# Optimization experiments

Hardware: AMD Instinct MI355X
Metric: run time of the kernel (lower is better)

## Reference

```python
import jax, jax.numpy as jnp
import numpy as np

N_NODES = 200000
N_EDGES = 6400000


def setup_inputs() -> dict:
    key = jax.random.key(0)
    ks = jax.random.split(key, 6)
    x = jax.random.normal(ks[0], (N_NODES, 11), dtype=jnp.float32)
    edge_index = jax.random.randint(ks[1], (2, N_EDGES), 0, N_NODES, dtype=jnp.int64)
    # orthogonal-ish init approximated by scaled gaussian; math path is identical
    W1 = jax.random.normal(ks[2], (11, 11), dtype=jnp.float32) / jnp.sqrt(11.0)
    W2 = jax.random.normal(ks[3], (11, 11), dtype=jnp.float32) / jnp.sqrt(11.0)
    W3 = jax.random.normal(ks[4], (11, 16), dtype=jnp.float32) / jnp.sqrt(11.0)
    b1 = jnp.zeros((11,), jnp.float32)
    b2 = jnp.zeros((11,), jnp.float32)
    b3 = jnp.zeros((16,), jnp.float32)
    return {"x": x, "edge_index": edge_index, "W1": W1, "b1": b1,
            "W2": W2, "b2": b2, "W3": W3, "b3": b3}


def gcn_conv(x, W, b, src, dst, n):
    """PyG GCNConv with add_self_loops=True, symmetric normalization.
    out_i = sum_{j->i} d_j^{-1/2} d_i^{-1/2} (x_j W) + d_i^{-1} (x_i W) + b
    where d includes the self-loop (+1).
    """
    h = x @ W                                                  # [N, F_out]
    deg = jax.ops.segment_sum(jnp.ones(src.shape[0], h.dtype), dst,
                              num_segments=n) + 1.0            # self-loop
    dinv = jax.lax.rsqrt(deg)                                  # [N]
    norm = dinv[src] * dinv[dst]                               # [E]
    agg = jax.ops.segment_sum(norm[:, None] * h[src], dst, num_segments=n)
    agg = agg + (dinv * dinv)[:, None] * h                     # self-loop term
    return agg + b


def reference(x, edge_index, W1, b1, W2, b2, W3, b3):
    n = x.shape[0]
    src, dst = edge_index[0], edge_index[1]
    h = jax.nn.relu(gcn_conv(x, W1, b1, src, dst, n))   # dropout p=0.0 -> identity
    h = jax.nn.relu(gcn_conv(h, W2, b2, src, dst, n))
    return gcn_conv(h, W3, b3, src, dst, n)
```

## Files before the change

kernel.cpp:

```cpp
#include <hip/hip_runtime.h>

#define N_NODES 200000
#define N_EDGES 6400000

constexpr int BSHIFT = 9;
constexpr int NBUCK  = (N_NODES + 511) / 512;
constexpr int CHUNK  = 16384;
constexpr int NCHUNK = (N_EDGES + CHUNK - 1) / CHUNK;
constexpr int MAXBUCK = 18432;
constexpr int SEGSTRIDE = 2052;
constexpr int SEGMAX = 1536;

__device__ __forceinline__ int ld_edge(const void* ei, int is64, int idx) {
    return is64 ? (int)((const long long*)ei)[idx] : ((const int*)ei)[idx];
}

__global__ void k_init(int* __restrict__ cursor, const unsigned int* __restrict__ ei,
                       int* __restrict__ flag, int* __restrict__ accG) {
    __shared__ int nz;
    int i = blockIdx.x * blockDim.x + threadIdx.x;
    if (i < N_NODES * 16) accG[i] = 0;
    if (blockIdx.x == 0) {
        int t = threadIdx.x;
        for (int j = t; j < NBUCK; j += 256) cursor[j] = j * MAXBUCK;
        if (t == 0) nz = 0;
        __syncthreads();
        if (ei[2 * t + 1] != 0u) atomicOr(&nz, 1);
        __syncthreads();
        if (t == 0) *flag = nz ? 0 : 1;
    }
}

__global__ void __launch_bounds__(1024)
k_binscatter(const void* __restrict__ ei, const int* __restrict__ flag,
             int* __restrict__ bucketCursor, unsigned int* __restrict__ bin) {
    __shared__ int hist[NBUCK];
    __shared__ int pref[NBUCK + 1];
    __shared__ int cur[NBUCK];
    __shared__ int gb[NBUCK];
    __shared__ int sc[512];
    __shared__ unsigned int stage[CHUNK];
    const int is64 = *flag;
    int b = blockIdx.x, t = threadIdx.x;
    int e0 = b * CHUNK;
    int n = min(CHUNK, N_EDGES - e0);
    for (int i = t; i < NBUCK; i += 1024) hist[i] = 0;
    int sd[16], ss[16];
#pragma unroll
    for (int j = 0; j < 16; ++j) {
        int idx = t + (j << 10);
        if (idx < n) {
            ss[j] = ld_edge(ei, is64, e0 + idx);
            sd[j] = ld_edge(ei, is64, N_EDGES + e0 + idx);
        } else {
            ss[j] = -1; sd[j] = -1;
        }
    }
    __syncthreads();
#pragma unroll
    for (int j = 0; j < 16; ++j)
        if (sd[j] >= 0) atomicAdd(&hist[sd[j] >> BSHIFT], 1);
    __syncthreads();
    if (t < 256) {
        sc[t]       = (t < NBUCK)       ? hist[t]       : 0;
        sc[t + 256] = (t + 256 < NBUCK) ? hist[t + 256] : 0;
    }
    __syncthreads();
    for (int off = 1; off < 512; off <<= 1) {
        int a0 = 0, a1 = 0;
        if (t < 256) {
            a0 = (t >= off) ? sc[t - off] : 0;
            a1 = sc[t + 256 - off];
        }
        __syncthreads();
        if (t < 256) { sc[t] += a0; sc[t + 256] += a1; }
        __syncthreads();
    }
    for (int i = t; i < NBUCK; i += 1024) {
        int excl = sc[i] - hist[i];
        pref[i] = excl;
        cur[i] = excl;
    }
    if (t == 0) pref[NBUCK] = n;
    __syncthreads();
#pragma unroll
    for (int j = 0; j < 16; ++j) {
        if (sd[j] >= 0) {
            int bk = sd[j] >> BSHIFT;
            unsigned int q = (unsigned int)ss[j] / 50000u;
            int p = atomicAdd(&cur[bk], 1);
            stage[p] = (q << 27) | ((unsigned int)(sd[j] & 511) << 18) | (unsigned int)ss[j];
        }
    }
    __syncthreads();
    for (int i = t; i < NBUCK; i += 1024) {
        int c = hist[i];
        gb[i] = c ? atomicAdd(&bucketCursor[i], c) : 0;
    }
    __syncthreads();
    int wave = t >> 6, lane = t & 63;
    for (int i = wave; i < NBUCK; i += 16) {
        int c = hist[i];
        if (!c) continue;
        int gg = gb[i];
        int room = (i + 1) * MAXBUCK - gg;
        int lim = min(c, max(room, 0));
        int pp = pref[i];
        for (int j = lane; j < lim; j += 64) bin[gg + j] = stage[pp + j];
    }
}

__global__ void __launch_bounds__(1024)
k_bucketsort(const int* __restrict__ bucketCursor, unsigned int* __restrict__ bin,
             float* __restrict__ dinv, unsigned short* __restrict__ seg16) {
    __shared__ int cnt[2048];
    __shared__ int cur[2048];
    __shared__ int tsum[1024];
    __shared__ unsigned int payload[MAXBUCK];
    int b = blockIdx.x, t = threadIdx.x;
    int base = b * MAXBUCK;
    int n = min(bucketCursor[b] - base, MAXBUCK);
    cnt[t] = 0; cnt[t + 1024] = 0;
    __syncthreads();
    for (int i = t; i < n; i += 1024) {
        unsigned int u = bin[base + i];
        int key = (int)((u >> 27) << 9) | (int)((u >> 18) & 511u);
        atomicAdd(&cnt[key], 1);
    }
    __syncthreads();
    int b0 = t * 2;
    int s = cnt[b0] + cnt[b0 + 1];
    tsum[t] = s;
    __syncthreads();
    int v = s;
    for (int off = 1; off < 1024; off <<= 1) {
        int add = (t >= off) ? tsum[t - off] : 0;
        __syncthreads();
        tsum[t] += add;
        __syncthreads();
    }
    int run = tsum[t] - v;
    cur[b0] = run;
    cur[b0 + 1] = run + cnt[b0];
    __syncthreads();
    for (int i = t; i < 2048; i += 1024)
        seg16[b * SEGSTRIDE + i] = (unsigned short)cur[i];
    if (t == 0) seg16[b * SEGSTRIDE + 2048] = (unsigned short)n;
    int node0 = b << BSHIFT;
    if (t < 512) {
        int node = node0 + t;
        if (node < N_NODES) {
            int deg = cnt[t] + cnt[512 + t] + cnt[1024 + t] + cnt[1536 + t];
            dinv[node] = rsqrtf((float)deg + 1.0f);
        }
    }
    __syncthreads();
    for (int i = t; i < n; i += 1024) {
        unsigned int u = bin[base + i];
        int key = (int)((u >> 27) << 9) | (int)((u >> 18) & 511u);
        int p = atomicAdd(&cur[key], 1);
        if (p < MAXBUCK) payload[p] = (u & 0x3FFFFu) << 4;
    }
    __syncthreads();
    for (int i = t; i < n; i += 1024) bin[base + i] = payload[i];
}

template <int FIN, int FOUT, int SIN>
__global__ void k_xw(const float* xin, const float* __restrict__ W,
                     const float* __restrict__ dinv, float* hs) {
    __shared__ float sW[FIN * FOUT];
    int t = threadIdx.x;
    if (t < FIN * FOUT) sW[t] = W[t];
    __syncthreads();
    int i = blockIdx.x * 256 + t;
    if (i >= N_NODES) return;
    float xi[FIN];
#pragma unroll
    for (int k = 0; k < FIN; ++k) xi[k] = xin[i * SIN + k];
    float di = dinv[i];
    float o[FOUT];
#pragma unroll
    for (int j = 0; j < FOUT; ++j) {
        float acc = 0.f;
#pragma unroll
        for (int k = 0; k < FIN; ++k) acc += xi[k] * sW[k * FOUT + j];
        o[j] = di * acc;
    }
#pragma unroll
    for (int j = 0; j < FOUT; ++j) hs[i * 16 + j] = o[j];
}

template <int FIN, int FOUT>
__global__ void k_fx(float* __restrict__ B, float* __restrict__ accG,
                     const float* __restrict__ dinv,
                     const float* __restrict__ biasPrev,
                     const float* __restrict__ Wnext) {
    __shared__ float sW[FIN * FOUT];
    __shared__ float sb[FIN];
    int t = threadIdx.x;
    if (t < FIN * FOUT) sW[t] = Wnext[t];
    if (t < FIN) sb[t] = biasPrev[t];
    __syncthreads();
    int i = blockIdx.x * 256 + t;
    if (i >= N_NODES) return;
    float di = dinv[i];
    float xi[FIN];
#pragma unroll
    for (int k = 0; k < FIN; ++k) {
        float v = di * (accG[i * 16 + k] + B[i * 16 + k]) + sb[k];
        xi[k] = fmaxf(v, 0.f);
    }
#pragma unroll
    for (int c = 0; c < 16; ++c) accG[i * 16 + c] = 0.f;
    float o[FOUT];
#pragma unroll
    for (int j = 0; j < FOUT; ++j) {
        float acc = 0.f;
#pragma unroll
        for (int k = 0; k < FIN; ++k) acc += xi[k] * sW[k * FOUT + j];
        o[j] = di * acc;
    }
#pragma unroll
    for (int j = 0; j < FOUT; ++j) B[i * 16 + j] = o[j];
}

__global__ void __launch_bounds__(512)
k_agg(const unsigned short* __restrict__ seg16,
      const unsigned int* __restrict__ bin, const float* __restrict__ hs,
      float* __restrict__ accG) {
    __shared__ unsigned short s_sr[132];
    __shared__ unsigned int s_bin[SEGMAX];
    int blk = blockIdx.x;
    int q = blk & 3;
    int Q = (blk >> 2) & 3;
    int b = blk >> 4;
    int t = threadIdx.x;
    int base = b * MAXBUCK;
    const unsigned short* sr = seg16 + b * SEGSTRIDE + (q << 9) + (Q << 7);
    if (t < 129) s_sr[t] = sr[t];
    __syncthreads();
    int s0 = (int)s_sr[0];
    int nseg = (int)s_sr[128] - s0;
    bool staged = (nseg <= SEGMAX);
    if (staged) {
        for (int i = t; i < nseg; i += 512) s_bin[i] = bin[base + s0 + i];
    }
    __syncthreads();
    int g = t >> 4, f = t & 15;
    int dd0 = g << 2;
    int r0 = (int)s_sr[dd0 + 0], r1 = (int)s_sr[dd0 + 1], r2 = (int)s_sr[dd0 + 2];
    int r3 = (int)s_sr[dd0 + 3], r4 = (int)s_sr[dd0 + 4];
    int n0 = r1 - r0, n1 = r2 - r1, n2 = r3 - r2, n3 = r4 - r3;
    float a0 = 0.f, a1 = 0.f, a2 = 0.f, a3 = 0.f;
    int m = max(max(n0, n1), max(n2, n3));
    if (staged) {
        int o0 = r0 - s0, o1 = r1 - s0, o2 = r2 - s0, o3 = r3 - s0;
#pragma unroll 2
        for (int k = 0; k < m; k += 2) {
            float t00 = 0.f, t01 = 0.f, t10 = 0.f, t11 = 0.f;
            float t20 = 0.f, t21 = 0.f, t30 = 0.f, t31 = 0.f;
            if (k     < n0) t00 = hs[s_bin[o0 + k]     + f];
            if (k + 1 < n0) t01 = hs[s_bin[o0 + k + 1] + f];
            if (k     < n1) t10 = hs[s_bin[o1 + k]     + f];
            if (k + 1 < n1) t11 = hs[s_bin[o1 + k + 1] + f];
            if (k     < n2) t20 = hs[s_bin[o2 + k]     + f];
            if (k + 1 < n2) t21 = hs[s_bin[o2 + k + 1] + f];
            if (k     < n3) t30 = hs[s_bin[o3 + k]     + f];
            if (k + 1 < n3) t31 = hs[s_bin[o3 + k + 1] + f];
            a0 += t00 + t01;
            a1 += t10 + t11;
            a2 += t20 + t21;
            a3 += t30 + t31;
        }
    } else {
        const unsigned int* p0 = bin + base + r0;
        const unsigned int* p1 = bin + base + r1;
        const unsigned int* p2 = bin + base + r2;
        const unsigned int* p3 = bin + base + r3;
#pragma unroll 2
        for (int k = 0; k < m; ++k) {
            if (k < n0) a0 += hs[p0[k] + f];
            if (k < n1) a1 += hs[p1[k] + f];
            if (k < n2) a2 += hs[p2[k] + f];
            if (k < n3) a3 += hs[p3[k] + f];
        }
    }
    int node0 = (b << BSHIFT) + (Q << 7) + dd0;
    if (node0 + 0 < N_NODES) unsafeAtomicAdd(&accG[((node0 + 0) << 4) + f], a0);
    if (node0 + 1 < N_NODES) unsafeAtomicAdd(&accG[((node0 + 1) << 4) + f], a1);
    if (node0 + 2 < N_NODES) unsafeAtomicAdd(&accG[((node0 + 2) << 4) + f], a2);
    if (node0 + 3 < N_NODES) unsafeAtomicAdd(&accG[((node0 + 3) << 4) + f], a3);
}

template <int F, bool RELU>
__global__ void k_finish(float* __restrict__ B, float* __restrict__ accG,
                         const float* __restrict__ dinv,
                         const float* __restrict__ bias, float* __restrict__ out) {
    int i = blockIdx.x * blockDim.x + threadIdx.x;
    if (i >= N_NODES * 16) return;
    int node = i >> 4, ff = i & 15;
    float di = dinv[node];
    if (ff < F) {
        float r = di * (accG[i] + B[i]) + bias[ff];
        if (RELU) r = fmaxf(r, 0.f);
        out[node * 16 + ff] = r;
    }
}

extern "C" void kernel_launch(void* const* d_in, const int* in_sizes, int n_in,
                              void* d_out, int out_size, void* d_ws, size_t ws_size,
                              hipStream_t stream) {
    const float* x  = (const float*)d_in[0];
    const void*  ei = d_in[1];
    const float* W1 = (const float*)d_in[2];
    const float* b1 = (const float*)d_in[3];
    const float* W2 = (const float*)d_in[4];
    const float* b2 = (const float*)d_in[5];
    const float* W3 = (const float*)d_in[6];
    const float* b3 = (const float*)d_in[7];
    float* out = (float*)d_out;

    char* w = (char*)d_ws;
    int*   bucketCursor = (int*)(w + 0);
    int*   flag         = (int*)(w + 2048);
    float* dinv         = (float*)(w + 2112);
    unsigned short* seg16 = (unsigned short*)(w + 802112);
    unsigned int* bin   = (unsigned int*)(w + 2406784);
    float* B            = (float*)(w + 31234432);
    float* accG         = out;

    k_init<<<12500, 256, 0, stream>>>(bucketCursor, (const unsigned int*)ei, flag, (int*)accG);
    k_binscatter<<<NCHUNK, 1024, 0, stream>>>(ei, flag, bucketCursor, bin);
    k_bucketsort<<<NBUCK, 1024, 0, stream>>>(bucketCursor, bin, dinv, seg16);

    k_xw<11, 11, 11><<<782, 256, 0, stream>>>(x, W1, dinv, B);
    k_agg<<<NBUCK * 16, 512, 0, stream>>>(seg16, bin, B, accG);
    k_fx<11, 11><<<782, 256, 0, stream>>>(B, accG, dinv, b1, W2);
    k_agg<<<NBUCK * 16, 512, 0, stream>>>(seg16, bin, B, accG);
    k_fx<11, 16><<<782, 256, 0, stream>>>(B, accG, dinv, b2, W3);
    k_agg<<<NBUCK * 16, 512, 0, stream>>>(seg16, bin, B, accG);
    k_finish<16, false><<<12500, 256, 0, stream>>>(B, accG, dinv, b3, out);
}
```

Baseline: 285.9 us.

## Sort destination nodes by in-degree within each bucket to balance aggregation

Within each bucket, the bucket sort now counting-sorts destination nodes by their (clamped) in-degree per quarter. It builds a permutation so that the four destinations handled by each 16-lane group have similar edge counts. The aggregation kernel loops to the max of four degrees, so this grouping is meant to cut wasted, predicated iterations and divergence. The cost is extra shared memory and passes in the bucket sort, a new permutation array in global memory, and scattered atomics to the permuted node addresses.

```diff
diff --git a/kernel.cpp b/kernel.cpp
--- a/kernel.cpp
+++ b/kernel.cpp
@@ -112,15 +112,21 @@
 
 __global__ void __launch_bounds__(1024)
 k_bucketsort(const int* __restrict__ bucketCursor, unsigned int* __restrict__ bin,
-             float* __restrict__ dinv, unsigned short* __restrict__ seg16) {
+             float* __restrict__ dinv, unsigned short* __restrict__ seg16,
+             unsigned short* __restrict__ permG) {
     __shared__ int cnt[2048];
+    __shared__ int cntP[2048];
     __shared__ int cur[2048];
     __shared__ int tsum[1024];
+    __shared__ int dhist[256];
+    __shared__ unsigned short rank[2048];
+    __shared__ unsigned short perm[2048];
     __shared__ unsigned int payload[MAXBUCK];
     int b = blockIdx.x, t = threadIdx.x;
     int base = b * MAXBUCK;
     int n = min(bucketCursor[b] - base, MAXBUCK);
     cnt[t] = 0; cnt[t + 1024] = 0;
+    if (t < 256) dhist[t] = 0;
     __syncthreads();
     for (int i = t; i < n; i += 1024) {
         unsigned int u = bin[base + i];
@@ -128,8 +134,30 @@
         atomicAdd(&cnt[key], 1);
     }
     __syncthreads();
+    for (int i = t; i < 2048; i += 1024) {
+        int dg = min(cnt[i], 63);
+        atomicAdd(&dhist[((i >> 9) << 6) | dg], 1);
+    }
+    __syncthreads();
+    if (t < 4) {
+        int acc = 0;
+        for (int j = 0; j < 64; ++j) {
+            int idx = (t << 6) | j;
+            int c = dhist[idx]; dhist[idx] = acc; acc += c;
+        }
+    }
+    __syncthreads();
+    for (int i = t; i < 2048; i += 1024) {
+        int dg = min(cnt[i], 63);
+        int q = i >> 9;
+        int r = atomicAdd(&dhist[(q << 6) | dg], 1);
+        rank[i] = (unsigned short)r;
+        perm[(q << 9) | r] = (unsigned short)(i & 511);
+        cntP[(q << 9) | r] = cnt[i];
+    }
+    __syncthreads();
     int b0 = t * 2;
-    int s = cnt[b0] + cnt[b0 + 1];
+    int s = cntP[b0] + cntP[b0 + 1];
     tsum[t] = s;
     __syncthreads();
     int v = s;
@@ -141,10 +169,12 @@
     }
     int run = tsum[t] - v;
     cur[b0] = run;
-    cur[b0 + 1] = run + cnt[b0];
-    __syncthreads();
-    for (int i = t; i < 2048; i += 1024)
+    cur[b0 + 1] = run + cntP[b0];
+    __syncthreads();
+    for (int i = t; i < 2048; i += 1024) {
         seg16[b * SEGSTRIDE + i] = (unsigned short)cur[i];
+        permG[b * 2048 + i] = perm[i];
+    }
     if (t == 0) seg16[b * SEGSTRIDE + 2048] = (unsigned short)n;
     int node0 = b << BSHIFT;
     if (t < 512) {
@@ -157,7 +187,8 @@
     __syncthreads();
     for (int i = t; i < n; i += 1024) {
         unsigned int u = bin[base + i];
-        int key = (int)((u >> 27) << 9) | (int)((u >> 18) & 511u);
+        int korig = (int)((u >> 27) << 9) | (int)((u >> 18) & 511u);
+        int key = (int)((u >> 27) << 9) | (int)rank[korig];
         int p = atomicAdd(&cur[key], 1);
         if (p < MAXBUCK) payload[p] = (u & 0x3FFFFu) << 4;
     }
@@ -225,10 +256,11 @@
 }
 
 __global__ void __launch_bounds__(512)
-k_agg(const unsigned short* __restrict__ seg16,
+k_agg(const unsigned short* __restrict__ seg16, const unsigned short* __restrict__ permG,
       const unsigned int* __restrict__ bin, const float* __restrict__ hs,
       float* __restrict__ accG) {
     __shared__ unsigned short s_sr[132];
+    __shared__ unsigned short s_perm[128];
     __shared__ unsigned int s_bin[SEGMAX];
     int blk = blockIdx.x;
     int q = blk & 3;
@@ -238,6 +270,7 @@
     int base = b * MAXBUCK;
     const unsigned short* sr = seg16 + b * SEGSTRIDE + (q << 9) + (Q << 7);
     if (t < 129) s_sr[t] = sr[t];
+    if (t >= 256 && t < 384) s_perm[t - 256] = permG[b * 2048 + (q << 9) + (Q << 7) + (t - 256)];
     __syncthreads();
     int s0 = (int)s_sr[0];
     int nseg = (int)s_sr[128] - s0;
@@ -285,11 +318,15 @@
             if (k < n3) a3 += hs[p3[k] + f];
         }
     }
-    int node0 = (b << BSHIFT) + (Q << 7) + dd0;
-    if (node0 + 0 < N_NODES) unsafeAtomicAdd(&accG[((node0 + 0) << 4) + f], a0);
-    if (node0 + 1 < N_NODES) unsafeAtomicAdd(&accG[((node0 + 1) << 4) + f], a1);
-    if (node0 + 2 < N_NODES) unsafeAtomicAdd(&accG[((node0 + 2) << 4) + f], a2);
-    if (node0 + 3 < N_NODES) unsafeAtomicAdd(&accG[((node0 + 3) << 4) + f], a3);
+    int node0 = b << BSHIFT;
+    int d0 = node0 + (int)s_perm[dd0 + 0];
+    int d1 = node0 + (int)s_perm[dd0 + 1];
+    int d2 = node0 + (int)s_perm[dd0 + 2];
+    int d3 = node0 + (int)s_perm[dd0 + 3];
+    if (d0 < N_NODES) unsafeAtomicAdd(&accG[(d0 << 4) + f], a0);
+    if (d1 < N_NODES) unsafeAtomicAdd(&accG[(d1 << 4) + f], a1);
+    if (d2 < N_NODES) unsafeAtomicAdd(&accG[(d2 << 4) + f], a2);
+    if (d3 < N_NODES) unsafeAtomicAdd(&accG[(d3 << 4) + f], a3);
 }
 
 template <int F, bool RELU>
@@ -325,19 +362,20 @@
     int*   flag         = (int*)(w + 2048);
     float* dinv         = (float*)(w + 2112);
     unsigned short* seg16 = (unsigned short*)(w + 802112);
-    unsigned int* bin   = (unsigned int*)(w + 2406784);
-    float* B            = (float*)(w + 31234432);
+    unsigned short* permG = (unsigned short*)(w + 2406784);
+    unsigned int* bin   = (unsigned int*)(w + 4008320);
+    float* B            = (float*)(w + 32835968);
     float* accG         = out;
 
     k_init<<<12500, 256, 0, stream>>>(bucketCursor, (const unsigned int*)ei, flag, (int*)accG);
     k_binscatter<<<NCHUNK, 1024, 0, stream>>>(ei, flag, bucketCursor, bin);
-    k_bucketsort<<<NBUCK, 1024, 0, stream>>>(bucketCursor, bin, dinv, seg16);
+    k_bucketsort<<<NBUCK, 1024, 0, stream>>>(bucketCursor, bin, dinv, seg16, permG);
 
     k_xw<11, 11, 11><<<782, 256, 0, stream>>>(x, W1, dinv, B);
-    k_agg<<<NBUCK * 16, 512, 0, stream>>>(seg16, bin, B, accG);
+    k_agg<<<NBUCK * 16, 512, 0, stream>>>(seg16, permG, bin, B, accG);
     k_fx<11, 11><<<782, 256, 0, stream>>>(B, accG, dinv, b1, W2);
-    k_agg<<<NBUCK * 16, 512, 0, stream>>>(seg16, bin, B, accG);
+    k_agg<<<NBUCK * 16, 512, 0, stream>>>(seg16, permG, bin, B, accG);
     k_fx<11, 16><<<782, 256, 0, stream>>>(B, accG, dinv, b2, W3);
-    k_agg<<<NBUCK * 16, 512, 0, stream>>>(seg16, bin, B, accG);
+    k_agg<<<NBUCK * 16, 512, 0, stream>>>(seg16, permG, bin, B, accG);
     k_finish<16, false><<<12500, 256, 0, stream>>>(B, accG, dinv, b3, out);
 }
```

Result: slower. 353.1 us (+23.5%).
